# Performance work log

Measured on AMD Instinct MI355X. Metric: run time of the kernel, lower is better.

## Reference

```python
import jax, jax.numpy as jnp
import numpy as np

DIM, NUM, S, W_RANK = 33, 20, 5, 20
EPS = 1e-5
MEAN = np.array([0.485, 0.456, 0.406], np.float32).reshape(1, 3, 1, 1)
STD = np.array([0.229, 0.224, 0.225], np.float32).reshape(1, 3, 1, 1)


def _conv_s2(x, w, b):
    y = jax.lax.conv_general_dilated(x, w, (2, 2), [(1, 1), (1, 1)],
                                     dimension_numbers=('NCHW', 'OIHW', 'NCHW'))
    return y + b[None, :, None, None]


def _inorm(x, g, b):
    m = jnp.mean(x, axis=(2, 3), keepdims=True)
    v = jnp.var(x, axis=(2, 3), keepdims=True)  # biased var, as torch InstanceNorm2d
    return (x - m) * jax.lax.rsqrt(v + EPS) * g[None, :, None, None] + b[None, :, None, None]


def _lrelu(x):
    return jnp.where(x >= 0, x, 0.2 * x)


def _hardswish(x):
    return x * jnp.clip(x + 3.0, 0.0, 6.0) * (1.0 / 6.0)


def _cube_to_lut(cube):  # cube: (num, 3, d, d, d); channel-own axis is first spatial axis
    lut_r = jnp.transpose(cube[:, 0], (0, 2, 3, 1))  # (r,b,g) -> (b,g,r)
    lut_g = jnp.transpose(cube[:, 1], (0, 2, 1, 3))  # (g,b,r) -> (b,g,r)
    lut_b = cube[:, 2]                               # already (b,g,r)
    return jnp.stack([lut_r, lut_g, lut_b], axis=1)  # (num, 3, b, g, r)


def _trilinear(lut, x):
    # lut: (3, d, d, d) indexed [c, b, g, r]; x: (3, H, W) with values in [0,1]
    d = lut.shape[-1]
    binsize = 1.000001 / (d - 1)  # matches CUDA kernel
    pos = x / binsize
    idx = jnp.clip(jnp.floor(pos).astype(jnp.int32), 0, d - 2)
    f = pos - idx
    r0, g0, b0 = idx[0], idx[1], idx[2]
    rd, gd, bd = f[0], f[1], f[2]
    r1, g1, b1 = r0 + 1, g0 + 1, b0 + 1
    out = (lut[:, b0, g0, r0] * ((1 - rd) * (1 - gd) * (1 - bd))
         + lut[:, b0, g0, r1] * (rd * (1 - gd) * (1 - bd))
         + lut[:, b0, g1, r0] * ((1 - rd) * gd * (1 - bd))
         + lut[:, b1, g0, r0] * ((1 - rd) * (1 - gd) * bd)
         + lut[:, b0, g1, r1] * (rd * gd * (1 - bd))
         + lut[:, b1, g0, r1] * (rd * (1 - gd) * bd)
         + lut[:, b1, g1, r0] * ((1 - rd) * gd * bd)
         + lut[:, b1, g1, r1] * (rd * gd * bd))
    return out  # (3, H, W)


def _forward(img, img_org,
             c0w, c0b, n0g, n0b, c1w, c1b, n1g, n1b,
             c2w, c2b, n2g, n2b, c3w, c3b, n3g, n3b,
             c4w, c4b, cls0_w, cls0_b, cls1_w, cls1_b,
             s_layers, w_layers, luts):
    x = (img - jnp.asarray(MEAN)) / jnp.asarray(STD)
    # BackBone: [Conv s2, LeakyReLU(0.2), InstanceNorm] x4, then Conv s2 + LeakyReLU
    x = _inorm(_lrelu(_conv_s2(x, c0w, c0b)), n0g, n0b)
    x = _inorm(_lrelu(_conv_s2(x, c1w, c1b)), n1g, n1b)
    x = _inorm(_lrelu(_conv_s2(x, c2w, c2b)), n2g, n2b)
    x = _inorm(_lrelu(_conv_s2(x, c3w, c3b)), n3g, n3b)
    x = _lrelu(_conv_s2(x, c4w, c4b))
    feat = jnp.mean(x, axis=(2, 3))  # AdaptiveAvgPool2d(1) -> (B, 128); Dropout=id (eval)
    # classifier (1x1 convs on 1x1 feature == dense layers)
    h = _hardswish(feat @ cls0_w.T + cls0_b)
    weight = h @ cls1_w.T + cls1_b  # (B, num)
    # CLUT '++' low-rank LUT reconstruction
    cube = (s_layers @ (luts @ w_layers).reshape(S, NUM * 3 * DIM * DIM))  # (dim, num*3*dim*dim)
    cube = cube.reshape(DIM, NUM * 3, DIM * DIM).transpose(1, 0, 2).reshape(NUM, 3, DIM, DIM, DIM)
    d3luts = _cube_to_lut(cube)  # (num, 3, d, d, d)
    d3lut = (weight @ d3luts.reshape(NUM, -1)).reshape(-1, 3, DIM, DIM, DIM)  # per-image LUT
    res = jax.vmap(_trilinear)(d3lut, img_org)  # (B, 3, H, W)
    return res + img_org


def setup_inputs() -> dict:
    key = jax.random.key(0)
    ks = jax.random.split(key, 24)
    chans = [3, 16, 32, 64, 128, 128]
    inp = {}
    inp['img'] = jax.random.uniform(ks[0], (8, 3, 256, 256), jnp.float32)
    inp['img_org'] = jax.random.uniform(ks[1], (8, 3, 720, 1280), jnp.float32)
    for i in range(5):
        cin, cout = chans[i], chans[i + 1]
        scale = 1.0 / np.sqrt(cin * 9)
        inp[f'c{i}w'] = jax.random.normal(ks[2 + i], (cout, cin, 3, 3), jnp.float32) * scale
        inp[f'c{i}b'] = jnp.zeros((cout,), jnp.float32)
    for i in range(4):
        inp[f'n{i}g'] = jnp.ones((chans[i + 1],), jnp.float32)
        inp[f'n{i}b'] = jnp.zeros((chans[i + 1],), jnp.float32)
    inp['cls0_w'] = jax.random.normal(ks[10], (128, 128), jnp.float32) * (1.0 / np.sqrt(128))
    inp['cls0_b'] = jnp.zeros((128,), jnp.float32)
    inp['cls1_w'] = jax.random.normal(ks[11], (NUM, 128), jnp.float32) * (1.0 / np.sqrt(128))
    inp['cls1_b'] = jnp.zeros((NUM,), jnp.float32)
    inp['s_layers'] = jax.random.uniform(ks[12], (DIM, S), jnp.float32) / 5.0 - 0.1
    inp['w_layers'] = jax.random.uniform(ks[13], (W_RANK, DIM * DIM), jnp.float32) / 5.0 - 0.1
    # torch init is zeros; use small random values for a non-degenerate test
    inp['luts'] = jax.random.normal(ks[14], (S * NUM * 3, W_RANK), jnp.float32) * 0.01
    return inp


def reference(img, img_org, c0w, c0b, n0g, n0b, c1w, c1b, n1g, n1b,
              c2w, c2b, n2g, n2b, c3w, c3b, n3g, n3b, c4w, c4b,
              cls0_w, cls0_b, cls1_w, cls1_b, s_layers, w_layers, luts):
    return _forward(img, img_org, c0w, c0b, n0g, n0b, c1w, c1b, n1g, n1b,
                    c2w, c2b, n2g, n2b, c3w, c3b, n3g, n3b, c4w, c4b,
                    cls0_w, cls0_b, cls1_w, cls1_b, s_layers, w_layers, luts)
```

## Files before the change

### kernel.cpp

```cpp
#include <hip/hip_runtime.h>
#include <hip/hip_fp16.h>

typedef _Float16 h2 __attribute__((ext_vector_type(2)));

constexpr size_t OFF_Y0    = 0;
constexpr size_t OFF_Y1    = 2097152;
constexpr size_t OFF_Y2    = 3145728;
constexpr size_t OFF_Y3    = 3670016;
constexpr size_t OFF_U     = 3670016;
constexpr size_t OFF_LUTC  = 0;
constexpr size_t OFF_LUTQ  = 1048576;
constexpr size_t OFF_STATB = 4926640;
constexpr size_t OFF_STAT0 = OFF_STATB + 0;
constexpr size_t OFF_STAT1 = OFF_STATB + 256;
constexpr size_t OFF_STAT2 = OFF_STATB + 768;
constexpr size_t OFF_STAT3 = OFF_STATB + 1792;
constexpr size_t OFF_FEATS = OFF_STATB + 3840;
constexpr size_t OFF_MAXB  = OFF_STATB + 4864;

__global__ __launch_bounds__(256) void zero_k(float* __restrict__ p, int n) {
  int i = blockIdx.x*256 + threadIdx.x;
  if (i < n) p[i] = 0.f;
}

template<int CIN, int COUT, int HIN, int WIN, int TH, int OCG, int PX, int OCT, int BLK>
__global__ __launch_bounds__(BLK) void conv_f32_first(
    const float* __restrict__ xin, const float* __restrict__ wgt,
    const float* __restrict__ bias,
    float* __restrict__ yout, float* __restrict__ stat_out)
{
  constexpr int HOUT = HIN/2, WOUT = WIN/2;
  constexpr int SEG  = WOUT + 4;
  constexpr int XROW = 2*SEG;
  constexpr int XPI  = (2*TH+1)*XROW;
  constexpr int NT   = HOUT/TH;
  constexpr int NSTRIP_B = TH*WOUT/PX;
  constexpr int GPT  = OCG/OCT;
  static_assert(BLK == NSTRIP_B*GPT, "thread mapping mismatch");
  constexpr int R = NSTRIP_B < 64 ? NSTRIP_B : 64;

  __shared__ __align__(16) float xs[CIN*XPI];
  __shared__ float s_sc[CIN], s_sf[CIN];

  const int tid = threadIdx.x;
  const int lin = blockIdx.x;
  const int b = lin & 7;
  const int r2 = lin >> 3;
  const int tile = r2 % NT;
  const int ocb  = r2 / NT;

  if (tid == 0)      { s_sc[0] = 1.f/0.229f; s_sf[0] = -0.485f/0.229f; }
  else if (tid == 1) { s_sc[1] = 1.f/0.224f; s_sf[1] = -0.456f/0.224f; }
  else if (tid == 2) { s_sc[2] = 1.f/0.225f; s_sf[2] = -0.406f/0.225f; }
  __syncthreads();

  const int iy0 = tile*(2*TH) - 1;
  const float* xb_g = xin + (size_t)b*CIN*HIN*WIN;
  for (int e = tid; e < CIN*(2*TH+1)*(WIN+2); e += BLK) {
    int ic  = e / ((2*TH+1)*(WIN+2));
    int rem = e - ic*((2*TH+1)*(WIN+2));
    int rr  = rem / (WIN+2);
    int cc  = rem - rr*(WIN+2);
    int iy = iy0 + rr, ix = cc - 1;
    float v = 0.f;
    if (iy >= 0 && iy < HIN && ix >= 0 && ix < WIN)
      v = s_sc[ic]*xb_g[(size_t)ic*HIN*WIN + iy*WIN + ix] + s_sf[ic];
    int off = (ix & 1) ? (SEG + ((ix+1) >> 1)) : (ix >> 1);
    xs[ic*XPI + rr*XROW + off] = v;
  }
  __syncthreads();

  const int s  = tid % NSTRIP_B;
  const int g  = tid / NSTRIP_B;
  const int r  = s / (WOUT/PX);
  const int c0 = (s % (WOUT/PX)) * PX;
  const int oc0 = ocb*OCG + g*OCT;

  float acc[OCT][PX];
  #pragma unroll
  for (int k = 0; k < OCT; ++k) {
    float bb = bias[oc0+k];
    #pragma unroll
    for (int j = 0; j < PX; ++j) acc[k][j] = bb;
  }

  for (int ic = 0; ic < CIN; ++ic) {
    float wv[OCT][9];
    #pragma unroll
    for (int k = 0; k < OCT; ++k) {
      const float* wp = wgt + ((size_t)(oc0+k)*CIN + ic)*9;
      #pragma unroll
      for (int t = 0; t < 9; ++t) wv[k][t] = wp[t];
    }
    const float* xb = xs + ic*XPI;
    #pragma unroll
    for (int ky = 0; ky < 3; ++ky) {
      const float* rowp = xb + (2*r+ky)*XROW;
      float eb[PX], ob[PX+1];
      static_assert(PX == 8, "conv0 uses PX=8");
      *(float4*)&eb[0] = *(const float4*)(rowp + c0);
      *(float4*)&eb[4] = *(const float4*)(rowp + c0 + 4);
      *(float4*)&ob[0] = *(const float4*)(rowp + SEG + c0);
      *(float4*)&ob[4] = *(const float4*)(rowp + SEG + c0 + 4);
      ob[8] = rowp[SEG + c0 + 8];
      #pragma unroll
      for (int k = 0; k < OCT; ++k) {
        float w0 = wv[k][ky*3], w1 = wv[k][ky*3+1], w2 = wv[k][ky*3+2];
        #pragma unroll
        for (int j = 0; j < PX; ++j)
          acc[k][j] += w0*ob[j] + w1*eb[j] + w2*ob[j+1];
      }
    }
  }

  const int oy = tile*TH + r;
  float lsum[OCT], lsq[OCT];
  #pragma unroll
  for (int k = 0; k < OCT; ++k) {
    float ov[PX];
    float ls = 0.f, lq = 0.f;
    #pragma unroll
    for (int j = 0; j < PX; ++j) {
      float a = acc[k][j];
      a = a >= 0.f ? a : 0.2f*a;
      ov[j] = a; ls += a; lq += a*a;
    }
    lsum[k] = ls; lsq[k] = lq;
    float* yp = yout + (((size_t)b*COUT + oc0 + k)*HOUT + oy)*WOUT + c0;
    *(float4*)yp = *(float4*)&ov[0];
    *(float4*)(yp+4) = *(float4*)&ov[4];
  }
  #pragma unroll
  for (int k = 0; k < OCT; ++k) {
    #pragma unroll
    for (int off = R/2; off > 0; off >>= 1) {
      lsum[k] += __shfl_down(lsum[k], off);
      lsq[k]  += __shfl_down(lsq[k],  off);
    }
  }
  if ((tid & (R-1)) == 0) {
    #pragma unroll
    for (int k = 0; k < OCT; ++k) {
      atomicAdd(&stat_out[(b*COUT + oc0 + k)*2 + 0], lsum[k]);
      atomicAdd(&stat_out[(b*COUT + oc0 + k)*2 + 1], lsq[k]);
    }
  }
}

template<int CIN, int COUT, int HIN, int WIN, int TH, int OCG, int PX, int OCT,
         int BLK, int MODE, int NPXPREV>
__global__ __launch_bounds__(BLK) void conv_h2(
    const float* __restrict__ xin, const float* __restrict__ wgt,
    const float* __restrict__ bias, const float* __restrict__ stat_in,
    const float* __restrict__ gam, const float* __restrict__ bet,
    float* __restrict__ yout, float* __restrict__ stat_out)
{
  constexpr int CINH = CIN/2;
  constexpr int HOUT = HIN/2, WOUT = WIN/2;
  constexpr int SEG  = WOUT + 4;
  constexpr int XROW = 2*SEG;
  constexpr int XPI  = (2*TH+1)*XROW;
  constexpr int NT   = HOUT/TH;
  constexpr int NSTRIP_B = TH*WOUT/PX;
  constexpr int GPT  = OCG/OCT;
  static_assert(BLK == NSTRIP_B*GPT, "thread mapping mismatch");
  constexpr int R = NSTRIP_B < 64 ? NSTRIP_B : 64;

  __shared__ __align__(16) h2 xs[CINH*XPI];
  __shared__ float s_sc[CIN], s_sf[CIN];

  const int tid = threadIdx.x;
  const int lin = blockIdx.x;
  const int b = lin & 7;
  const int r2 = lin >> 3;
  const int tile = r2 % NT;
  const int ocb  = r2 / NT;

  if (tid < CIN) {
    float S = stat_in[(b*CIN+tid)*2+0], Q = stat_in[(b*CIN+tid)*2+1];
    float mean = S*(1.0f/NPXPREV);
    float var  = Q*(1.0f/NPXPREV) - mean*mean;
    float rstd = rsqrtf(var + 1e-5f);
    float gg = gam[tid], bb = bet[tid];
    s_sc[tid] = gg*rstd;
    s_sf[tid] = bb - mean*gg*rstd;
  }
  __syncthreads();

  const int iy0 = tile*(2*TH) - 1;
  const float* xb_g = xin + (size_t)b*CIN*HIN*WIN;
  for (int e = tid; e < CINH*(2*TH+1)*(WIN+2); e += BLK) {
    int icp = e / ((2*TH+1)*(WIN+2));
    int rem = e - icp*((2*TH+1)*(WIN+2));
    int rr  = rem / (WIN+2);
    int cc  = rem - rr*(WIN+2);
    int iy = iy0 + rr, ix = cc - 1;
    float v0 = 0.f, v1 = 0.f;
    if (iy >= 0 && iy < HIN && ix >= 0 && ix < WIN) {
      int ic0 = 2*icp;
      v0 = s_sc[ic0]  *xb_g[(size_t)ic0*HIN*WIN + iy*WIN + ix]     + s_sf[ic0];
      v1 = s_sc[ic0+1]*xb_g[(size_t)(ic0+1)*HIN*WIN + iy*WIN + ix] + s_sf[ic0+1];
    }
    int off = (ix & 1) ? (SEG + ((ix+1) >> 1)) : (ix >> 1);
    h2 p; p[0] = (_Float16)v0; p[1] = (_Float16)v1;
    xs[icp*XPI + rr*XROW + off] = p;
  }
  __syncthreads();

  const int s  = tid % NSTRIP_B;
  const int g  = tid / NSTRIP_B;
  const int r  = s / (WOUT/PX);
  const int c0 = (s % (WOUT/PX)) * PX;
  const int oc0 = ocb*OCG + g*OCT;

  float acc[OCT][PX];
  #pragma unroll
  for (int k = 0; k < OCT; ++k) {
    float bb = bias[oc0+k];
    #pragma unroll
    for (int j = 0; j < PX; ++j) acc[k][j] = bb;
  }

  for (int icp = 0; icp < CINH; ++icp) {
    h2 wv[OCT][9];
    #pragma unroll
    for (int k = 0; k < OCT; ++k) {
      const float* wp0 = wgt + ((size_t)(oc0+k)*CIN + 2*icp)*9;
      const float* wp1 = wp0 + 9;
      #pragma unroll
      for (int t = 0; t < 9; ++t) {
        h2 w; w[0] = (_Float16)wp0[t]; w[1] = (_Float16)wp1[t];
        wv[k][t] = w;
      }
    }
    const h2* xb = xs + icp*XPI;
    #pragma unroll
    for (int ky = 0; ky < 3; ++ky) {
      const h2* rowp = xb + (2*r+ky)*XROW;
      h2 eb[PX], ob[PX+1];
      if constexpr (PX == 4) {
        *(uint4*)&eb[0] = *(const uint4*)(rowp + c0);
        *(uint4*)&ob[0] = *(const uint4*)(rowp + SEG + c0);
        ob[4] = rowp[SEG + c0 + 4];
      } else if constexpr (PX == 2) {
        *(uint2*)&eb[0] = *(const uint2*)(rowp + c0);
        *(uint2*)&ob[0] = *(const uint2*)(rowp + SEG + c0);
        ob[2] = rowp[SEG + c0 + 2];
      } else {
        eb[0] = rowp[c0];
        ob[0] = rowp[SEG + c0];
        ob[1] = rowp[SEG + c0 + 1];
      }
      #pragma unroll
      for (int k = 0; k < OCT; ++k) {
        h2 w0 = wv[k][ky*3], w1 = wv[k][ky*3+1], w2 = wv[k][ky*3+2];
        #pragma unroll
        for (int j = 0; j < PX; ++j) {
          float a = acc[k][j];
          a = __builtin_amdgcn_fdot2(w0, ob[j],   a, false);
          a = __builtin_amdgcn_fdot2(w1, eb[j],   a, false);
          a = __builtin_amdgcn_fdot2(w2, ob[j+1], a, false);
          acc[k][j] = a;
        }
      }
    }
  }

  const int oy = tile*TH + r;
  if constexpr (MODE != 2) {
    float lsum[OCT], lsq[OCT];
    #pragma unroll
    for (int k = 0; k < OCT; ++k) {
      float ov[PX];
      float ls = 0.f, lq = 0.f;
      #pragma unroll
      for (int j = 0; j < PX; ++j) {
        float a = acc[k][j];
        a = a >= 0.f ? a : 0.2f*a;
        ov[j] = a; ls += a; lq += a*a;
      }
      lsum[k] = ls; lsq[k] = lq;
      float* yp = yout + (((size_t)b*COUT + oc0 + k)*HOUT + oy)*WOUT + c0;
      if constexpr (PX == 4) {
        *(float4*)yp = *(float4*)&ov[0];
      } else if constexpr (PX == 2) {
        *(float2*)yp = *(float2*)&ov[0];
      } else {
        *yp = ov[0];
      }
    }
    #pragma unroll
    for (int k = 0; k < OCT; ++k) {
      #pragma unroll
      for (int off = R/2; off > 0; off >>= 1) {
        lsum[k] += __shfl_down(lsum[k], off);
        lsq[k]  += __shfl_down(lsq[k],  off);
      }
    }
    if ((tid & (R-1)) == 0) {
      #pragma unroll
      for (int k = 0; k < OCT; ++k) {
        atomicAdd(&stat_out[(b*COUT + oc0 + k)*2 + 0], lsum[k]);
        atomicAdd(&stat_out[(b*COUT + oc0 + k)*2 + 1], lsq[k]);
      }
    }
  } else {
    float a = acc[0][0];
    a = a >= 0.f ? a : 0.2f*a;
    #pragma unroll
    for (int off = R/2; off > 0; off >>= 1) a += __shfl_down(a, off);
    if ((tid & (R-1)) == 0) atomicAdd(&stat_out[b*COUT + oc0], a);
  }
}

__global__ __launch_bounds__(256) void u_direct_kernel(
    const float* __restrict__ featsum, const float* __restrict__ w0, const float* __restrict__ b0,
    const float* __restrict__ w1, const float* __restrict__ b1,
    const float* __restrict__ luts, const float* __restrict__ wl, float* __restrict__ U)
{
  __shared__ float sh_h[128];
  __shared__ float sh_w[20];
  __shared__ float sh_v[20];
  const int tid = threadIdx.x;
  const int lin = blockIdx.x;
  const int bt = lin & 7;
  const int rest = lin >> 3;
  const int j = rest / 5, qb = rest % 5;
  const int s = j / 3, ch = j % 3;

  if (tid < 128) {
    const float* f = featsum + bt*128;
    const float* w = w0 + tid*128;
    float a = 0.f;
    for (int k = 0; k < 128; ++k) a += f[k]*w[k];
    a = b0[tid] + a*(1.0f/64.0f);
    float c = fminf(fmaxf(a + 3.f, 0.f), 6.f);
    sh_h[tid] = a * c * (1.f/6.f);
  }
  __syncthreads();
  if (tid < 20) {
    const float* w = w1 + tid*128;
    float a = b1[tid];
    for (int k = 0; k < 128; ++k) a += sh_h[k]*w[k];
    sh_w[tid] = a;
  }
  __syncthreads();
  if (tid < 20) {
    float a = 0.f;
    #pragma unroll
    for (int n = 0; n < 20; ++n)
      a += sh_w[n] * luts[(s*60 + n*3 + ch)*20 + tid];
    sh_v[tid] = a;
  }
  __syncthreads();
  const int q = qb*256 + tid;
  if (q < 1089) {
    float a = 0.f;
    #pragma unroll
    for (int w = 0; w < 20; ++w) a += sh_v[w] * wl[w*1089 + q];
    U[(size_t)(bt*15 + j)*1089 + q] = a;
  }
}

__global__ __launch_bounds__(256) void lutc_max_kernel(
    const float* __restrict__ U, const float* __restrict__ slay,
    uint2* __restrict__ lutc, unsigned* __restrict__ maxbuf)
{
  __shared__ float s_slay[165];
  __shared__ unsigned s_max;
  const int tid = threadIdx.x;
  if (tid < 165) s_slay[tid] = slay[tid];
  if (tid == 0) s_max = 0u;
  __syncthreads();
  const int lin = blockIdx.x;
  const int bt = lin & 7;
  const int i = (lin >> 3)*256 + tid;
  if (i < 35937) {
    int bi = i / 1089, rem = i - bi*1089, gi = rem / 33, ri = rem - gi*33;
    const float* Ub = U + (size_t)bt*15*1089;
    float v0 = 0.f, v1 = 0.f, v2 = 0.f;
    #pragma unroll
    for (int s = 0; s < 5; ++s) {
      v0 += s_slay[ri*5+s] * Ub[(s*3+0)*1089 + bi*33 + gi];
      v1 += s_slay[gi*5+s] * Ub[(s*3+1)*1089 + bi*33 + ri];
      v2 += s_slay[bi*5+s] * Ub[(s*3+2)*1089 + gi*33 + ri];
    }
    union { __half2 h2v; unsigned u; } p0, p1;
    p0.h2v = __floats2half2_rn(v0, v1);
    p1.h2v = __floats2half2_rn(v2, 0.f);
    lutc[(size_t)bt*35937 + i] = make_uint2(p0.u, p1.u);
    float m = fmaxf(fmaxf(fabsf(v0), fabsf(v1)), fabsf(v2));
    atomicMax(&s_max, __float_as_uint(m));
  }
  __syncthreads();
  if (tid == 0) atomicMax(&maxbuf[bt], s_max);
}

__global__ __launch_bounds__(256) void lutq_kernel(
    const uint2* __restrict__ lutc, const unsigned* __restrict__ maxbuf,
    unsigned* __restrict__ lutq)
{
  const int lin = blockIdx.x;
  const int bt = lin & 7;
  const int i = (lin >> 3)*256 + threadIdx.x;
  if (i >= 35937) return;
  float maxv = __uint_as_float(maxbuf[bt]);
  float enc = maxv > 0.f ? 511.0f/maxv : 0.f;
  uint2 c = lutc[(size_t)bt*35937 + i];
  __half2 h01 = *(__half2*)&c.x;
  __half2 h2_ = *(__half2*)&c.y;
  float v0 = __low2float(h01), v1 = __high2float(h01), v2 = __low2float(h2_);
  int q0 = (int)rintf(v0*enc) + 512;
  int q1 = (int)rintf(v1*enc) + 512;
  int q2 = (int)rintf(v2*enc) + 512;
  q0 = q0 < 0 ? 0 : (q0 > 1023 ? 1023 : q0);
  q1 = q1 < 0 ? 0 : (q1 > 1023 ? 1023 : q1);
  q2 = q2 < 0 ? 0 : (q2 > 1023 ? 1023 : q2);
  lutq[(size_t)bt*35937 + i] = (unsigned)q0 | ((unsigned)q1 << 10) | ((unsigned)q2 << 20);
}

__device__ __forceinline__ void pair_acc(unsigned ca, unsigned cb, float wp, float fr,
                                         float& a0, float& a1, float& a2)
{
  float q0a = (float)(ca & 1023u), q1a = (float)((ca >> 10) & 1023u), q2a = (float)((ca >> 20) & 1023u);
  float q0b = (float)(cb & 1023u), q1b = (float)((cb >> 10) & 1023u), q2b = (float)((cb >> 20) & 1023u);
  a0 += wp * (q0a + fr*(q0b - q0a));
  a1 += wp * (q1a + fr*(q1b - q1a));
  a2 += wp * (q2a + fr*(q2b - q2a));
}

__global__ __launch_bounds__(1024) void trilin_lds_kernel(
    const float* __restrict__ img, const unsigned* __restrict__ lutq,
    const unsigned* __restrict__ maxbuf, float* __restrict__ out)
{
  constexpr int NPX = 720*1280;
  constexpr int NV4 = NPX/4;
  constexpr int PER_BLK = NV4/32;
  __shared__ unsigned s_lut[35937];

  const int tid = threadIdx.x;
  const int lin = blockIdx.x;
  const int bt = lin & 7;
  const int bb = lin >> 3;
  const unsigned* Lg = lutq + (size_t)bt*35937;
  for (int i = tid; i < 35937; i += 1024) s_lut[i] = Lg[i];
  __syncthreads();

  const float maxv  = __uint_as_float(maxbuf[bt]);
  const float scale = maxv * (1.0f/511.0f);
  const float offc  = -512.0f * scale;
  const float* ib = img + (size_t)bt*3*NPX;
  float* ob = out + (size_t)bt*3*NPX;
  const float invbin = 32.0f/1.000001f;
  const int vend = bb*PER_BLK + PER_BLK;

  for (int v = bb*PER_BLK + tid; v < vend; v += 1024) {
    float4 r4 = ((const float4*)ib)[v];
    float4 g4 = ((const float4*)(ib + NPX))[v];
    float4 b4 = ((const float4*)(ib + 2*NPX))[v];
    float4 ro, go, bo;
    float* rp = (float*)&ro; float* gp = (float*)&go; float* bp = (float*)&bo;
    #pragma unroll
    for (int j = 0; j < 4; ++j) {
      float r = ((float*)&r4)[j], g = ((float*)&g4)[j], b = ((float*)&b4)[j];
      float pr = r*invbin, pg = g*invbin, pb = b*invbin;
      int ri = (int)pr; ri = ri > 31 ? 31 : ri; ri = ri < 0 ? 0 : ri;
      int gi = (int)pg; gi = gi > 31 ? 31 : gi; gi = gi < 0 ? 0 : gi;
      int bi = (int)pb; bi = bi > 31 ? 31 : bi; bi = bi < 0 ? 0 : bi;
      float fr = pr - ri, fg = pg - gi, fb = pb - bi;
      int i00 = (bi*33 + gi)*33 + ri;
      unsigned c00a = s_lut[i00],        c00b = s_lut[i00 + 1];
      unsigned c01a = s_lut[i00 + 33],   c01b = s_lut[i00 + 34];
      unsigned c10a = s_lut[i00 + 1089], c10b = s_lut[i00 + 1090];
      unsigned c11a = s_lut[i00 + 1122], c11b = s_lut[i00 + 1123];
      float wb0 = 1.f - fb, wb1 = fb, wg0 = 1.f - fg, wg1 = fg;
      float a0 = 0.f, a1 = 0.f, a2 = 0.f;
      pair_acc(c00a, c00b, wb0*wg0, fr, a0, a1, a2);
      pair_acc(c01a, c01b, wb0*wg1, fr, a0, a1, a2);
      pair_acc(c10a, c10b, wb1*wg0, fr, a0, a1, a2);
      pair_acc(c11a, c11b, wb1*wg1, fr, a0, a1, a2);
      rp[j] = a0*scale + offc + r;
      gp[j] = a1*scale + offc + g;
      bp[j] = a2*scale + offc + b;
    }
    ((float4*)ob)[v]           = ro;
    ((float4*)(ob + NPX))[v]   = go;
    ((float4*)(ob + 2*NPX))[v] = bo;
  }
}

extern "C" void kernel_launch(void* const* d_in, const int* in_sizes, int n_in,
                              void* d_out, int out_size, void* d_ws, size_t ws_size,
                              hipStream_t stream) {
  const float* img     = (const float*)d_in[0];
  const float* img_org = (const float*)d_in[1];
  const float* c0w = (const float*)d_in[2];  const float* c0b = (const float*)d_in[3];
  const float* c1w = (const float*)d_in[4];  const float* c1b = (const float*)d_in[5];
  const float* c2w = (const float*)d_in[6];  const float* c2b = (const float*)d_in[7];
  const float* c3w = (const float*)d_in[8];  const float* c3b = (const float*)d_in[9];
  const float* c4w = (const float*)d_in[10]; const float* c4b = (const float*)d_in[11];
  const float* n0g = (const float*)d_in[12]; const float* n0b = (const float*)d_in[13];
  const float* n1g = (const float*)d_in[14]; const float* n1b = (const float*)d_in[15];
  const float* n2g = (const float*)d_in[16]; const float* n2b = (const float*)d_in[17];
  const float* n3g = (const float*)d_in[18]; const float* n3b = (const float*)d_in[19];
  const float* cls0_w = (const float*)d_in[20]; const float* cls0_b = (const float*)d_in[21];
  const float* cls1_w = (const float*)d_in[22]; const float* cls1_b = (const float*)d_in[23];
  const float* s_layers = (const float*)d_in[24];
  const float* w_layers = (const float*)d_in[25];
  const float* luts     = (const float*)d_in[26];
  float* ws = (float*)d_ws;
  float* out = (float*)d_out;

  zero_k<<<20, 256, 0, stream>>>(ws + OFF_STATB, 4872);

  conv_f32_first<3,16,256,256, 4,16, 8,2, 512><<<256, 512, 0, stream>>>(
      img, c0w, c0b, ws + OFF_Y0, ws + OFF_STAT0);
  conv_h2<16,32,128,128, 2,32, 4,2, 512, 1, 16384><<<256, 512, 0, stream>>>(
      ws + OFF_Y0, c1w, c1b, ws + OFF_STAT0, n0g, n0b, ws + OFF_Y1, ws + OFF_STAT1);
  conv_h2<32,64,64,64, 2,32, 2,2, 512, 1, 4096><<<256, 512, 0, stream>>>(
      ws + OFF_Y1, c2w, c2b, ws + OFF_STAT1, n1g, n1b, ws + OFF_Y2, ws + OFF_STAT2);
  conv_h2<64,128,32,32, 2,32, 1,2, 512, 1, 1024><<<256, 512, 0, stream>>>(
      ws + OFF_Y2, c3w, c3b, ws + OFF_STAT2, n2g, n2b, ws + OFF_Y3, ws + OFF_STAT3);
  conv_h2<128,128,16,16, 2,16, 1,1, 256, 2, 256><<<256, 256, 0, stream>>>(
      ws + OFF_Y3, c4w, c4b, ws + OFF_STAT3, n3g, n3b, nullptr, ws + OFF_FEATS);

  u_direct_kernel<<<600, 256, 0, stream>>>(
      ws + OFF_FEATS, cls0_w, cls0_b, cls1_w, cls1_b,
      luts, w_layers, ws + OFF_U);

  lutc_max_kernel<<<141*8, 256, 0, stream>>>(
      ws + OFF_U, s_layers, (uint2*)(ws + OFF_LUTC), (unsigned*)(ws + OFF_MAXB));

  lutq_kernel<<<141*8, 256, 0, stream>>>(
      (const uint2*)(ws + OFF_LUTC), (const unsigned*)(ws + OFF_MAXB),
      (unsigned*)(ws + OFF_LUTQ));

  trilin_lds_kernel<<<256, 1024, 0, stream>>>(
      img_org, (const unsigned*)(ws + OFF_LUTQ), (const unsigned*)(ws + OFF_MAXB), out);
}
```

Measured before the change: 193.5 us.

## Store intermediate conv activations as fp16 channel pairs instead of fp32

The conv layers now write their outputs as packed half2 pairs of adjacent channels, and the next layer reads one h2 per pixel instead of two separate fp32 channel planes. This halves activation write and read traffic between the backbone stages. The workspace offsets are moved to fit the new layout. Statistics are still computed from the fp32 values, but the stored activations lose precision before normalization, although the consumer already converted them to fp16 in LDS.

Result: no change. 190.9 us (-1.3%).

```diff
diff --git a/kernel.cpp b/kernel.cpp
--- a/kernel.cpp
+++ b/kernel.cpp
@@ -7,9 +7,9 @@
 constexpr size_t OFF_Y1    = 2097152;
 constexpr size_t OFF_Y2    = 3145728;
 constexpr size_t OFF_Y3    = 3670016;
-constexpr size_t OFF_U     = 3670016;
-constexpr size_t OFF_LUTC  = 0;
-constexpr size_t OFF_LUTQ  = 1048576;
+constexpr size_t OFF_U     = 3670016 + 65536;
+constexpr size_t OFF_LUTC  = 1048576;
+constexpr size_t OFF_LUTQ  = 2400000;
 constexpr size_t OFF_STATB = 4926640;
 constexpr size_t OFF_STAT0 = OFF_STATB + 0;
 constexpr size_t OFF_STAT1 = OFF_STATB + 256;
@@ -27,7 +27,7 @@
 __global__ __launch_bounds__(BLK) void conv_f32_first(
     const float* __restrict__ xin, const float* __restrict__ wgt,
     const float* __restrict__ bias,
-    float* __restrict__ yout, float* __restrict__ stat_out)
+    h2* __restrict__ yout, float* __restrict__ stat_out)
 {
   constexpr int HOUT = HIN/2, WOUT = WIN/2;
   constexpr int SEG  = WOUT + 4;
@@ -37,6 +37,7 @@
   constexpr int NSTRIP_B = TH*WOUT/PX;
   constexpr int GPT  = OCG/OCT;
   static_assert(BLK == NSTRIP_B*GPT, "thread mapping mismatch");
+  static_assert(OCT == 2, "pair write");
   constexpr int R = NSTRIP_B < 64 ? NSTRIP_B : 64;
 
   __shared__ __align__(16) float xs[CIN*XPI];
@@ -114,22 +115,26 @@
   }
 
   const int oy = tile*TH + r;
+  float ov[OCT][PX];
   float lsum[OCT], lsq[OCT];
   #pragma unroll
   for (int k = 0; k < OCT; ++k) {
-    float ov[PX];
     float ls = 0.f, lq = 0.f;
     #pragma unroll
     for (int j = 0; j < PX; ++j) {
       float a = acc[k][j];
       a = a >= 0.f ? a : 0.2f*a;
-      ov[j] = a; ls += a; lq += a*a;
+      ov[k][j] = a; ls += a; lq += a*a;
     }
     lsum[k] = ls; lsq[k] = lq;
-    float* yp = yout + (((size_t)b*COUT + oc0 + k)*HOUT + oy)*WOUT + c0;
-    *(float4*)yp = *(float4*)&ov[0];
-    *(float4*)(yp+4) = *(float4*)&ov[4];
-  }
+  }
+  h2 ph[PX];
+  #pragma unroll
+  for (int j = 0; j < PX; ++j) { ph[j][0] = (_Float16)ov[0][j]; ph[j][1] = (_Float16)ov[1][j]; }
+  h2* yp = yout + (((size_t)b*(COUT/2) + (oc0 >> 1))*HOUT + oy)*WOUT + c0;
+  *(uint4*)yp       = *(uint4*)&ph[0];
+  *(uint4*)(yp + 4) = *(uint4*)&ph[4];
+
   #pragma unroll
   for (int k = 0; k < OCT; ++k) {
     #pragma unroll
@@ -150,10 +155,10 @@
 template<int CIN, int COUT, int HIN, int WIN, int TH, int OCG, int PX, int OCT,
          int BLK, int MODE, int NPXPREV>
 __global__ __launch_bounds__(BLK) void conv_h2(
-    const float* __restrict__ xin, const float* __restrict__ wgt,
+    const h2* __restrict__ xin, const float* __restrict__ wgt,
     const float* __restrict__ bias, const float* __restrict__ stat_in,
     const float* __restrict__ gam, const float* __restrict__ bet,
-    float* __restrict__ yout, float* __restrict__ stat_out)
+    h2* __restrict__ yout, float* __restrict__ stat_out)
 {
   constexpr int CINH = CIN/2;
   constexpr int HOUT = HIN/2, WOUT = WIN/2;
@@ -164,6 +169,7 @@
   constexpr int NSTRIP_B = TH*WOUT/PX;
   constexpr int GPT  = OCG/OCT;
   static_assert(BLK == NSTRIP_B*GPT, "thread mapping mismatch");
+  static_assert(OCT == 2 || MODE == 2, "pair write needs OCT=2");
   constexpr int R = NSTRIP_B < 64 ? NSTRIP_B : 64;
 
   __shared__ __align__(16) h2 xs[CINH*XPI];
@@ -188,7 +194,7 @@
   __syncthreads();
 
   const int iy0 = tile*(2*TH) - 1;
-  const float* xb_g = xin + (size_t)b*CIN*HIN*WIN;
+  const h2* xb_g = xin + (size_t)b*CINH*HIN*WIN;
   for (int e = tid; e < CINH*(2*TH+1)*(WIN+2); e += BLK) {
     int icp = e / ((2*TH+1)*(WIN+2));
     int rem = e - icp*((2*TH+1)*(WIN+2));
@@ -197,9 +203,10 @@
     int iy = iy0 + rr, ix = cc - 1;
     float v0 = 0.f, v1 = 0.f;
     if (iy >= 0 && iy < HIN && ix >= 0 && ix < WIN) {
+      h2 x = xb_g[(size_t)icp*HIN*WIN + iy*WIN + ix];
       int ic0 = 2*icp;
-      v0 = s_sc[ic0]  *xb_g[(size_t)ic0*HIN*WIN + iy*WIN + ix]     + s_sf[ic0];
-      v1 = s_sc[ic0+1]*xb_g[(size_t)(ic0+1)*HIN*WIN + iy*WIN + ix] + s_sf[ic0+1];
+      v0 = s_sc[ic0]  *(float)x[0] + s_sf[ic0];
+      v1 = s_sc[ic0+1]*(float)x[1] + s_sf[ic0+1];
     }
     int off = (ix & 1) ? (SEG + ((ix+1) >> 1)) : (ix >> 1);
     h2 p; p[0] = (_Float16)v0; p[1] = (_Float16)v1;
@@ -268,26 +275,29 @@
 
   const int oy = tile*TH + r;
   if constexpr (MODE != 2) {
+    float ov[OCT][PX];
     float lsum[OCT], lsq[OCT];
     #pragma unroll
     for (int k = 0; k < OCT; ++k) {
-      float ov[PX];
       float ls = 0.f, lq = 0.f;
       #pragma unroll
       for (int j = 0; j < PX; ++j) {
         float a = acc[k][j];
         a = a >= 0.f ? a : 0.2f*a;
-        ov[j] = a; ls += a; lq += a*a;
+        ov[k][j] = a; ls += a; lq += a*a;
       }
       lsum[k] = ls; lsq[k] = lq;
-      float* yp = yout + (((size_t)b*COUT + oc0 + k)*HOUT + oy)*WOUT + c0;
-      if constexpr (PX == 4) {
-        *(float4*)yp = *(float4*)&ov[0];
-      } else if constexpr (PX == 2) {
-        *(float2*)yp = *(float2*)&ov[0];
-      } else {
-        *yp = ov[0];
-      }
+    }
+    h2 ph[PX];
+    #pragma unroll
+    for (int j = 0; j < PX; ++j) { ph[j][0] = (_Float16)ov[0][j]; ph[j][1] = (_Float16)ov[1][j]; }
+    h2* yp = yout + (((size_t)b*(COUT/2) + (oc0 >> 1))*HOUT + oy)*WOUT + c0;
+    if constexpr (PX == 4) {
+      *(uint4*)yp = *(uint4*)&ph[0];
+    } else if constexpr (PX == 2) {
+      *(uint2*)yp = *(uint2*)&ph[0];
+    } else {
+      yp[0] = ph[0];
     }
     #pragma unroll
     for (int k = 0; k < OCT; ++k) {
@@ -514,15 +524,19 @@
   zero_k<<<20, 256, 0, stream>>>(ws + OFF_STATB, 4872);
 
   conv_f32_first<3,16,256,256, 4,16, 8,2, 512><<<256, 512, 0, stream>>>(
-      img, c0w, c0b, ws + OFF_Y0, ws + OFF_STAT0);
+      img, c0w, c0b, (h2*)(ws + OFF_Y0), ws + OFF_STAT0);
   conv_h2<16,32,128,128, 2,32, 4,2, 512, 1, 16384><<<256, 512, 0, stream>>>(
-      ws + OFF_Y0, c1w, c1b, ws + OFF_STAT0, n0g, n0b, ws + OFF_Y1, ws + OFF_STAT1);
+      (const h2*)(ws + OFF_Y0), c1w, c1b, ws + OFF_STAT0, n0g, n0b,
+      (h2*)(ws + OFF_Y1), ws + OFF_STAT1);
   conv_h2<32,64,64,64, 2,32, 2,2, 512, 1, 4096><<<256, 512, 0, stream>>>(
-      ws + OFF_Y1, c2w, c2b, ws + OFF_STAT1, n1g, n1b, ws + OFF_Y2, ws + OFF_STAT2);
+      (const h2*)(ws + OFF_Y1), c2w, c2b, ws + OFF_STAT1, n1g, n1b,
+      (h2*)(ws + OFF_Y2), ws + OFF_STAT2);
   conv_h2<64,128,32,32, 2,32, 1,2, 512, 1, 1024><<<256, 512, 0, stream>>>(
-      ws + OFF_Y2, c3w, c3b, ws + OFF_STAT2, n2g, n2b, ws + OFF_Y3, ws + OFF_STAT3);
+      (const h2*)(ws + OFF_Y2), c3w, c3b, ws + OFF_STAT2, n2g, n2b,
+      (h2*)(ws + OFF_Y3), ws + OFF_STAT3);
   conv_h2<128,128,16,16, 2,16, 1,1, 256, 2, 256><<<256, 256, 0, stream>>>(
-      ws + OFF_Y3, c4w, c4b, ws + OFF_STAT3, n3g, n3b, nullptr, ws + OFF_FEATS);
+      (const h2*)(ws + OFF_Y3), c4w, c4b, ws + OFF_STAT3, n3g, n3b,
+      nullptr, ws + OFF_FEATS);
 
   u_direct_kernel<<<600, 256, 0, stream>>>(
       ws + OFF_FEATS, cls0_w, cls0_b, cls1_w, cls1_b,
```
